# Performance work log

Hardware: AMD Instinct MI355X
Metric: run time of the kernel (lower is better)

Reference implementation:

```python
import jax, jax.numpy as jnp
import numpy as np

PS = 32

def _masks(ps):
    yy, xx = np.meshgrid(np.arange(ps), np.arange(ps), indexing='ij')
    c = (ps - 1) / 2.0
    r = np.sqrt((yy - c) ** 2 + (xx - c) ** 2)
    rm = max(r.max(), 1.0)
    ml = (r <= rm / 3.0).astype(np.float32)
    mm = ((r > rm / 3.0) & (r <= 2.0 * rm / 3.0)).astype(np.float32)
    mh = (r > 2.0 * rm / 3.0).astype(np.float32)
    return jnp.asarray(ml), jnp.asarray(mm), jnp.asarray(mh)

MASK_L, MASK_M, MASK_H = _masks(PS)

def setup_inputs() -> dict:
    key = jax.random.key(0)
    ks = jax.random.split(key, 4)
    B, C, H, W = 16, 3, 256, 256
    d = PS * PS            # 1024
    hidden = int(d * 1.5)  # 1536
    c_f = 64
    return {
        'x': jax.random.normal(ks[0], (B, C, H, W), dtype=jnp.float32),
        'W1': jax.random.normal(ks[1], (d, hidden), dtype=jnp.float32) * 0.02,
        'b1': jnp.zeros((hidden,), jnp.float32),
        'W2': jax.random.normal(ks[2], (hidden, d), dtype=jnp.float32) * 0.02,
        'b2': jnp.zeros((d,), jnp.float32),
        'w_proj': jax.random.normal(ks[3], (c_f,), dtype=jnp.float32) * 0.5,
        'gamma': jnp.ones((c_f,), jnp.float32),
        'beta': jnp.zeros((c_f,), jnp.float32),
        'lf_gate': jnp.float32(0.33),
        'mf_gate': jnp.float32(0.34),
        'hf_gate': jnp.float32(0.33),
    }

def _forward(x, W1, b1, W2, b2, w_proj, gamma, beta, lf_gate, mf_gate, hf_gate):
    B, C, H, W = x.shape
    ps = PS
    gh, gw = H // ps, W // ps
    L = gh * gw
    # grayscale
    xg = 0.299 * x[:, 0] + 0.587 * x[:, 1] + 0.114 * x[:, 2]  # [B,H,W]
    # non-overlapping patchify (H,W multiples of ps -> no padding)
    pr = xg.reshape(B, gh, ps, gw, ps).transpose(0, 1, 3, 2, 4).reshape(B, L, ps, ps)
    # per-patch orthonormal FFT2 and magnitude
    mag = jnp.abs(jnp.fft.fft2(pr, norm='ortho'))  # [B,L,ps,ps]
    gate = (jax.nn.sigmoid(lf_gate) * MASK_L
            + jax.nn.sigmoid(mf_gate) * MASK_M
            + jax.nn.sigmoid(hf_gate) * MASK_H)
    mag = mag * gate
    mag_vec = mag.reshape(B * L, ps * ps)
    attn = jax.nn.sigmoid(jax.nn.relu(mag_vec @ W1 + b1) @ W2 + b2)
    mod = mag_vec * attn
    w = mod.mean(axis=-1).reshape(B, L, 1, 1)  # per-patch scalar weight
    recon = pr * (1.0 + w)
    # fold back (exact inverse of the reshape patchify)
    x_rec = recon.reshape(B, gh, gw, ps, ps).transpose(0, 1, 3, 2, 4).reshape(B, H, W)
    # 1x1 conv (1 -> c_f channels, no bias)
    out = x_rec[:, None, :, :] * w_proj[None, :, None, None]  # [B,c_f,H,W]
    # BatchNorm2d (training mode: batch stats, biased variance)
    mean = out.mean(axis=(0, 2, 3), keepdims=True)
    var = out.var(axis=(0, 2, 3), keepdims=True)
    out = (out - mean) * jax.lax.rsqrt(var + 1e-5)
    out = out * gamma[None, :, None, None] + beta[None, :, None, None]
    return jax.nn.relu(out)

def reference(x, W1, b1, W2, b2, w_proj, gamma, beta, lf_gate, mf_gate, hf_gate):
    return _forward(x, W1, b1, W2, b2, w_proj, gamma, beta, lf_gate, mf_gate, hf_gate)
```

## Files before the change

### kernel.cpp

```cpp
#include <hip/hip_runtime.h>
#include <hip/hip_bf16.h>
#include <math.h>

typedef __attribute__((ext_vector_type(8))) short bf16x8;
typedef __attribute__((ext_vector_type(4))) float f32x4;
typedef __attribute__((ext_vector_type(4))) unsigned short u16x4;

static __device__ __forceinline__ float bf2f(unsigned short u) {
    union { unsigned int i; float f; } v; v.i = ((unsigned int)u) << 16; return v.f;
}
static __device__ __forceinline__ unsigned short f2bf(float f) {
    union { float f; unsigned int i; } v; v.f = f;
    unsigned int x = v.i;
    return (unsigned short)((x + 0x7fffu + ((x >> 16) & 1u)) >> 16);
}
static __device__ __forceinline__ float sigmoidf(float v) {
    return 1.0f / (1.0f + expf(-v));
}

__global__ __launch_bounds__(256) void kpatch(
    const float* __restrict__ x, const float* __restrict__ lf,
    const float* __restrict__ mf, const float* __restrict__ hf,
    float* __restrict__ pr_out, unsigned short* __restrict__ mag_bf)
{
    __shared__ float sX[32][36];
    __shared__ float sYr[32][36];
    __shared__ float sYi[32][36];
    __shared__ float tc[32], ts[32];

    const int t = threadIdx.x;
    const int p = blockIdx.x;
    const int b = p >> 6, l = p & 63;
    const int gy = l >> 3, gx = l & 7;

    if (t < 32) {
        float ang = (float)t * 0.19634954084936207f;
        tc[t] = cosf(ang);
        ts[t] = sinf(ang);
    }

    const int y  = t >> 3;
    const int xc = (t & 7) * 4;
    const int h  = gy * 32 + y;
    const int wbase = gx * 32 + xc;
    const long long idx0 = ((long long)(b * 3 + 0) * 256 + h) * 256 + wbase;
    const long long idx1 = ((long long)(b * 3 + 1) * 256 + h) * 256 + wbase;
    const long long idx2 = ((long long)(b * 3 + 2) * 256 + h) * 256 + wbase;
    float4 r4 = *(const float4*)(x + idx0);
    float4 g4 = *(const float4*)(x + idx1);
    float4 b4 = *(const float4*)(x + idx2);
    float4 gray;
    gray.x = 0.299f * r4.x + 0.587f * g4.x + 0.114f * b4.x;
    gray.y = 0.299f * r4.y + 0.587f * g4.y + 0.114f * b4.y;
    gray.z = 0.299f * r4.z + 0.587f * g4.z + 0.114f * b4.z;
    gray.w = 0.299f * r4.w + 0.587f * g4.w + 0.114f * b4.w;
    *(float4*)&sX[y][xc] = gray;
    *(float4*)(pr_out + p * 1024 + t * 4) = gray;
    __syncthreads();

    {
        const int k  = t >> 3;
        const int c0 = (t & 7) * 4;
        float yr[4] = {0,0,0,0}, yi[4] = {0,0,0,0};
        for (int n = 0; n < 32; n++) {
            int wi = (k * n) & 31;
            float cw = tc[wi], sw = ts[wi];
            float4 xv = *(const float4*)&sX[n][c0];
            yr[0] += cw * xv.x; yi[0] -= sw * xv.x;
            yr[1] += cw * xv.y; yi[1] -= sw * xv.y;
            yr[2] += cw * xv.z; yi[2] -= sw * xv.z;
            yr[3] += cw * xv.w; yi[3] -= sw * xv.w;
        }
        *(float4*)&sYr[k][c0] = *(float4*)yr;
        *(float4*)&sYi[k][c0] = *(float4*)yi;
    }
    __syncthreads();

    {
        const int k  = t >> 3;
        const int m0 = (t & 7) * 4;
        float zr[4] = {0,0,0,0}, zi[4] = {0,0,0,0};
        for (int c = 0; c < 32; c++) {
            float yr = sYr[k][c];
            float yi = sYi[k][c];
            #pragma unroll
            for (int j = 0; j < 4; j++) {
                int wi = ((m0 + j) * c) & 31;
                float cw = tc[wi], sw = ts[wi];
                zr[j] += yr * cw + yi * sw;
                zi[j] += yi * cw - yr * sw;
            }
        }
        const float sl = sigmoidf(lf[0]);
        const float sm = sigmoidf(mf[0]);
        const float sh = sigmoidf(hf[0]);
        const float T1 = 480.5f / 9.0f;
        const float T2 = 4.0f * 480.5f / 9.0f;
        const float fk = (float)k - 15.5f;
        u16x4 outv;
        #pragma unroll
        for (int j = 0; j < 4; j++) {
            float fm = (float)(m0 + j) - 15.5f;
            float r2 = fk * fk + fm * fm;
            float g = (r2 <= T1) ? sl : ((r2 <= T2) ? sm : sh);
            float magv = sqrtf(zr[j] * zr[j] + zi[j] * zi[j]) * 0.03125f * g;
            outv[j] = f2bf(magv);
        }
        *(u16x4*)(mag_bf + p * 1024 + k * 32 + m0) = outv;
    }
}

__global__ __launch_bounds__(256) void kconv(
    const float* __restrict__ W, unsigned short* __restrict__ WT, int K, int N)
{
    __shared__ float tile[32][33];
    const int k0 = blockIdx.x * 32, n0 = blockIdx.y * 32;
    const int tx = threadIdx.x & 31, ty = threadIdx.x >> 5;
    #pragma unroll
    for (int i = 0; i < 4; i++) {
        int r = ty + i * 8;
        tile[r][tx] = W[(long long)(k0 + r) * N + n0 + tx];
    }
    __syncthreads();
    #pragma unroll
    for (int i = 0; i < 4; i++) {
        int r = ty + i * 8;
        WT[(long long)(n0 + r) * K + k0 + tx] = f2bf(tile[tx][r]);
    }
}

__global__ __launch_bounds__(256) void kgemm(
    const unsigned short* __restrict__ A, const unsigned short* __restrict__ BT,
    const float* __restrict__ bias, unsigned short* __restrict__ C,
    int K, int N, int act)
{
    const int lane = threadIdx.x & 63;
    const int wave = threadIdx.x >> 6;
    const int wm = wave & 1, wn = wave >> 1;
    const int m_base = blockIdx.x * 64 + wm * 32;
    const int n_base = blockIdx.y * 64 + wn * 32;
    const int lr = lane & 15;
    const int koff = (lane >> 4) * 8;

    const unsigned short* pa0 = A  + (long long)(m_base + lr) * K + koff;
    const unsigned short* pa1 = pa0 + (long long)16 * K;
    const unsigned short* pb0 = BT + (long long)(n_base + lr) * K + koff;
    const unsigned short* pb1 = pb0 + (long long)16 * K;

    f32x4 acc00 = {0,0,0,0}, acc01 = {0,0,0,0}, acc10 = {0,0,0,0}, acc11 = {0,0,0,0};

    for (int kk = 0; kk < K; kk += 32) {
        bf16x8 a0 = *(const bf16x8*)(pa0 + kk);
        bf16x8 a1 = *(const bf16x8*)(pa1 + kk);
        bf16x8 b0 = *(const bf16x8*)(pb0 + kk);
        bf16x8 b1 = *(const bf16x8*)(pb1 + kk);
        acc00 = __builtin_amdgcn_mfma_f32_16x16x32_bf16(a0, b0, acc00, 0, 0, 0);
        acc01 = __builtin_amdgcn_mfma_f32_16x16x32_bf16(a0, b1, acc01, 0, 0, 0);
        acc10 = __builtin_amdgcn_mfma_f32_16x16x32_bf16(a1, b0, acc10, 0, 0, 0);
        acc11 = __builtin_amdgcn_mfma_f32_16x16x32_bf16(a1, b1, acc11, 0, 0, 0);
    }

    const int quad = lane >> 4;
    const int col0 = n_base + lr, col1 = col0 + 16;
    const float bias0 = bias[col0], bias1 = bias[col1];
    const int row0b = m_base + quad * 4;
    #pragma unroll
    for (int r = 0; r < 4; r++) {
        int row0 = row0b + r, row1 = row0 + 16;
        float v00 = acc00[r] + bias0;
        float v01 = acc01[r] + bias1;
        float v10 = acc10[r] + bias0;
        float v11 = acc11[r] + bias1;
        if (act == 0) {
            v00 = fmaxf(v00, 0.0f); v01 = fmaxf(v01, 0.0f);
            v10 = fmaxf(v10, 0.0f); v11 = fmaxf(v11, 0.0f);
        } else {
            v00 = sigmoidf(v00); v01 = sigmoidf(v01);
            v10 = sigmoidf(v10); v11 = sigmoidf(v11);
        }
        C[(long long)row0 * N + col0] = f2bf(v00);
        C[(long long)row0 * N + col1] = f2bf(v01);
        C[(long long)row1 * N + col0] = f2bf(v10);
        C[(long long)row1 * N + col1] = f2bf(v11);
    }
}

__global__ __launch_bounds__(256) void kmod(
    const unsigned short* __restrict__ mag_bf, const unsigned short* __restrict__ attn_bf,
    const float* __restrict__ pr, float* __restrict__ xrec, float* __restrict__ stats)
{
    __shared__ float red[8];
    __shared__ float sscale;
    const int t = threadIdx.x, p = blockIdx.x;
    const int lane = t & 63, wave = t >> 6;

    u16x4 mv = *(const u16x4*)(mag_bf + p * 1024 + t * 4);
    u16x4 av = *(const u16x4*)(attn_bf + p * 1024 + t * 4);
    float acc = bf2f(mv[0]) * bf2f(av[0]) + bf2f(mv[1]) * bf2f(av[1])
              + bf2f(mv[2]) * bf2f(av[2]) + bf2f(mv[3]) * bf2f(av[3]);
    #pragma unroll
    for (int off = 32; off > 0; off >>= 1) acc += __shfl_down(acc, off, 64);
    if (lane == 0) red[wave] = acc;
    __syncthreads();
    if (t == 0) {
        float s = red[0] + red[1] + red[2] + red[3];
        sscale = 1.0f + s * (1.0f / 1024.0f);
    }
    __syncthreads();
    const float sc = sscale;

    const int b = p >> 6, l = p & 63;
    const int gy = l >> 3, gx = l & 7;
    const int y = t >> 3, xc = (t & 7) * 4;
    float4 pv = *(const float4*)(pr + p * 1024 + t * 4);
    float4 rv;
    rv.x = pv.x * sc; rv.y = pv.y * sc; rv.z = pv.z * sc; rv.w = pv.w * sc;
    *(float4*)(xrec + (long long)b * 65536 + (gy * 32 + y) * 256 + gx * 32 + xc) = rv;

    float ls = rv.x + rv.y + rv.z + rv.w;
    float lq = rv.x * rv.x + rv.y * rv.y + rv.z * rv.z + rv.w * rv.w;
    #pragma unroll
    for (int off = 32; off > 0; off >>= 1) {
        ls += __shfl_down(ls, off, 64);
        lq += __shfl_down(lq, off, 64);
    }
    __syncthreads();
    if (lane == 0) red[wave] = ls;
    __syncthreads();
    float bs = (t == 0) ? (red[0] + red[1] + red[2] + red[3]) : 0.0f;
    __syncthreads();
    if (lane == 0) red[wave] = lq;
    __syncthreads();
    if (t == 0) {
        float bq = red[0] + red[1] + red[2] + red[3];
        atomicAdd(&stats[0], bs);
        atomicAdd(&stats[1], bq);
    }
}

__global__ void kstats(const float* __restrict__ stats, const float* __restrict__ w_proj,
                       const float* __restrict__ gamma, const float* __restrict__ beta,
                       float* __restrict__ der)
{
    const int c = threadIdx.x;
    const float invN = 1.0f / 1048576.0f;
    float mu  = stats[0] * invN;
    float var = stats[1] * invN - mu * mu;
    float wp = w_proj[c];
    float A = wp * gamma[c] / sqrtf(wp * wp * var + 1e-5f);
    der[c]      = A;
    der[64 + c] = beta[c];
    if (c == 0) der[128] = mu;
}

__global__ __launch_bounds__(256) void kout(
    const float* __restrict__ xrec, const float* __restrict__ der, float* __restrict__ out)
{
    const int i4 = blockIdx.x * 256 + threadIdx.x;
    const int plane = i4 >> 14;
    const int c = plane & 63;
    const int b = plane >> 6;
    const float A  = der[c];
    const float be = der[64 + c];
    const float mu = der[128];
    float4 v = ((const float4*)xrec)[b * 16384 + (i4 & 16383)];
    float4 o;
    o.x = fmaxf(fmaf(A, v.x - mu, be), 0.0f);
    o.y = fmaxf(fmaf(A, v.y - mu, be), 0.0f);
    o.z = fmaxf(fmaf(A, v.z - mu, be), 0.0f);
    o.w = fmaxf(fmaf(A, v.w - mu, be), 0.0f);
    ((float4*)out)[i4] = o;
}

extern "C" void kernel_launch(void* const* d_in, const int* in_sizes, int n_in,
                              void* d_out, int out_size, void* d_ws, size_t ws_size,
                              hipStream_t stream)
{
    const float* x      = (const float*)d_in[0];
    const float* W1     = (const float*)d_in[1];
    const float* b1     = (const float*)d_in[2];
    const float* W2     = (const float*)d_in[3];
    const float* b2     = (const float*)d_in[4];
    const float* w_proj = (const float*)d_in[5];
    const float* gamma  = (const float*)d_in[6];
    const float* beta   = (const float*)d_in[7];
    const float* lf     = (const float*)d_in[8];
    const float* mf     = (const float*)d_in[9];
    const float* hf     = (const float*)d_in[10];

    char* ws = (char*)d_ws;
    float* pr                 = (float*)(ws);
    float* xrec               = (float*)(ws + 4194304);
    unsigned short* mag_bf    = (unsigned short*)(ws + 8388608);
    unsigned short* attn_bf   = (unsigned short*)(ws + 10485760);
    unsigned short* hidden_bf = (unsigned short*)(ws + 12582912);
    unsigned short* w1t       = (unsigned short*)(ws + 15728640);
    unsigned short* w2t       = (unsigned short*)(ws + 18874368);
    float* stats              = (float*)(ws + 22020096);
    float* der                = (float*)(ws + 22020224);

    hipMemsetAsync(stats, 0, 8, stream);

    kconv<<<dim3(32, 48), 256, 0, stream>>>(W1, w1t, 1024, 1536);
    kconv<<<dim3(48, 32), 256, 0, stream>>>(W2, w2t, 1536, 1024);
    kpatch<<<1024, 256, 0, stream>>>(x, lf, mf, hf, pr, mag_bf);
    kgemm<<<dim3(16, 24), 256, 0, stream>>>(mag_bf, w1t, b1, hidden_bf, 1024, 1536, 0);
    kgemm<<<dim3(16, 16), 256, 0, stream>>>(hidden_bf, w2t, b2, attn_bf, 1536, 1024, 1);
    kmod<<<1024, 256, 0, stream>>>(mag_bf, attn_bf, pr, xrec, stats);
    kstats<<<1, 64, 0, stream>>>(stats, w_proj, gamma, beta, der);
    kout<<<65536, 256, 0, stream>>>(xrec, der, (float*)d_out);
}
```

Measured before the change: 398.0 us.

## Fuse attention dot-product into GEMM2 epilogue and drop xrec/kmod pass

```diff
diff --git a/kernel.cpp b/kernel.cpp
--- a/kernel.cpp
+++ b/kernel.cpp
@@ -21,17 +21,20 @@
 __global__ __launch_bounds__(256) void kpatch(
     const float* __restrict__ x, const float* __restrict__ lf,
     const float* __restrict__ mf, const float* __restrict__ hf,
-    float* __restrict__ pr_out, unsigned short* __restrict__ mag_bf)
+    float* __restrict__ pr_out, unsigned short* __restrict__ mag_bf,
+    float* __restrict__ ppsum, float* __restrict__ ppsq)
 {
     __shared__ float sX[32][36];
     __shared__ float sYr[32][36];
     __shared__ float sYi[32][36];
     __shared__ float tc[32], ts[32];
+    __shared__ float red_s[4], red_q[4];
 
     const int t = threadIdx.x;
     const int p = blockIdx.x;
     const int b = p >> 6, l = p & 63;
     const int gy = l >> 3, gx = l & 7;
+    const int lane = t & 63, wave = t >> 6;
 
     if (t < 32) {
         float ang = (float)t * 0.19634954084936207f;
@@ -56,7 +59,20 @@
     gray.w = 0.299f * r4.w + 0.587f * g4.w + 0.114f * b4.w;
     *(float4*)&sX[y][xc] = gray;
     *(float4*)(pr_out + p * 1024 + t * 4) = gray;
+
+    float ls = gray.x + gray.y + gray.z + gray.w;
+    float lq = gray.x * gray.x + gray.y * gray.y + gray.z * gray.z + gray.w * gray.w;
+    #pragma unroll
+    for (int off = 32; off > 0; off >>= 1) {
+        ls += __shfl_down(ls, off, 64);
+        lq += __shfl_down(lq, off, 64);
+    }
+    if (lane == 0) { red_s[wave] = ls; red_q[wave] = lq; }
     __syncthreads();
+    if (t == 0) {
+        ppsum[p] = red_s[0] + red_s[1] + red_s[2] + red_s[3];
+        ppsq[p]  = red_q[0] + red_q[1] + red_q[2] + red_q[3];
+    }
 
     {
         const int k  = t >> 3;
@@ -129,11 +145,11 @@
     }
 }
 
-__global__ __launch_bounds__(256) void kgemm(
+__global__ __launch_bounds__(256) void kgemm1(
     const unsigned short* __restrict__ A, const unsigned short* __restrict__ BT,
-    const float* __restrict__ bias, unsigned short* __restrict__ C,
-    int K, int N, int act)
-{
+    const float* __restrict__ bias, unsigned short* __restrict__ C)
+{
+    const int K = 1024, N = 1536;
     const int lane = threadIdx.x & 63;
     const int wave = threadIdx.x >> 6;
     const int wm = wave & 1, wn = wave >> 1;
@@ -167,109 +183,155 @@
     #pragma unroll
     for (int r = 0; r < 4; r++) {
         int row0 = row0b + r, row1 = row0 + 16;
-        float v00 = acc00[r] + bias0;
-        float v01 = acc01[r] + bias1;
-        float v10 = acc10[r] + bias0;
-        float v11 = acc11[r] + bias1;
-        if (act == 0) {
-            v00 = fmaxf(v00, 0.0f); v01 = fmaxf(v01, 0.0f);
-            v10 = fmaxf(v10, 0.0f); v11 = fmaxf(v11, 0.0f);
-        } else {
-            v00 = sigmoidf(v00); v01 = sigmoidf(v01);
-            v10 = sigmoidf(v10); v11 = sigmoidf(v11);
-        }
-        C[(long long)row0 * N + col0] = f2bf(v00);
-        C[(long long)row0 * N + col1] = f2bf(v01);
-        C[(long long)row1 * N + col0] = f2bf(v10);
-        C[(long long)row1 * N + col1] = f2bf(v11);
-    }
-}
-
-__global__ __launch_bounds__(256) void kmod(
-    const unsigned short* __restrict__ mag_bf, const unsigned short* __restrict__ attn_bf,
-    const float* __restrict__ pr, float* __restrict__ xrec, float* __restrict__ stats)
-{
-    __shared__ float red[8];
-    __shared__ float sscale;
-    const int t = threadIdx.x, p = blockIdx.x;
-    const int lane = t & 63, wave = t >> 6;
-
-    u16x4 mv = *(const u16x4*)(mag_bf + p * 1024 + t * 4);
-    u16x4 av = *(const u16x4*)(attn_bf + p * 1024 + t * 4);
-    float acc = bf2f(mv[0]) * bf2f(av[0]) + bf2f(mv[1]) * bf2f(av[1])
-              + bf2f(mv[2]) * bf2f(av[2]) + bf2f(mv[3]) * bf2f(av[3]);
-    #pragma unroll
-    for (int off = 32; off > 0; off >>= 1) acc += __shfl_down(acc, off, 64);
-    if (lane == 0) red[wave] = acc;
+        C[(long long)row0 * N + col0] = f2bf(fmaxf(acc00[r] + bias0, 0.0f));
+        C[(long long)row0 * N + col1] = f2bf(fmaxf(acc01[r] + bias1, 0.0f));
+        C[(long long)row1 * N + col0] = f2bf(fmaxf(acc10[r] + bias0, 0.0f));
+        C[(long long)row1 * N + col1] = f2bf(fmaxf(acc11[r] + bias1, 0.0f));
+    }
+}
+
+__global__ __launch_bounds__(256) void kgemm2d(
+    const unsigned short* __restrict__ A, const unsigned short* __restrict__ BT,
+    const float* __restrict__ bias, const unsigned short* __restrict__ mag,
+    float* __restrict__ wpart)
+{
+    const int K = 1536;
+    const int lane = threadIdx.x & 63;
+    const int wave = threadIdx.x >> 6;
+    const int wm = wave & 1, wn = wave >> 1;
+    const int m_base = blockIdx.x * 64 + wm * 32;
+    const int n_base = blockIdx.y * 64 + wn * 32;
+    const int lr = lane & 15;
+    const int koff = (lane >> 4) * 8;
+
+    const unsigned short* pa0 = A  + (long long)(m_base + lr) * K + koff;
+    const unsigned short* pa1 = pa0 + (long long)16 * K;
+    const unsigned short* pb0 = BT + (long long)(n_base + lr) * K + koff;
+    const unsigned short* pb1 = pb0 + (long long)16 * K;
+
+    f32x4 acc00 = {0,0,0,0}, acc01 = {0,0,0,0}, acc10 = {0,0,0,0}, acc11 = {0,0,0,0};
+
+    for (int kk = 0; kk < K; kk += 32) {
+        bf16x8 a0 = *(const bf16x8*)(pa0 + kk);
+        bf16x8 a1 = *(const bf16x8*)(pa1 + kk);
+        bf16x8 b0 = *(const bf16x8*)(pb0 + kk);
+        bf16x8 b1 = *(const bf16x8*)(pb1 + kk);
+        acc00 = __builtin_amdgcn_mfma_f32_16x16x32_bf16(a0, b0, acc00, 0, 0, 0);
+        acc01 = __builtin_amdgcn_mfma_f32_16x16x32_bf16(a0, b1, acc01, 0, 0, 0);
+        acc10 = __builtin_amdgcn_mfma_f32_16x16x32_bf16(a1, b0, acc10, 0, 0, 0);
+        acc11 = __builtin_amdgcn_mfma_f32_16x16x32_bf16(a1, b1, acc11, 0, 0, 0);
+    }
+
+    const int quad = lane >> 4;
+    const int col0 = n_base + lr, col1 = col0 + 16;
+    const float bias0 = bias[col0], bias1 = bias[col1];
+    const int row0b = m_base + quad * 4;
+
+    float dsum0[4], dsum1[4];
+    #pragma unroll
+    for (int r = 0; r < 4; r++) {
+        int row0 = row0b + r, row1 = row0 + 16;
+        float v00 = sigmoidf(acc00[r] + bias0);
+        float v01 = sigmoidf(acc01[r] + bias1);
+        float v10 = sigmoidf(acc10[r] + bias0);
+        float v11 = sigmoidf(acc11[r] + bias1);
+        float m00 = bf2f(mag[(long long)row0 * 1024 + col0]);
+        float m01 = bf2f(mag[(long long)row0 * 1024 + col1]);
+        float m10 = bf2f(mag[(long long)row1 * 1024 + col0]);
+        float m11 = bf2f(mag[(long long)row1 * 1024 + col1]);
+        dsum0[r] = m00 * v00 + m01 * v01;
+        dsum1[r] = m10 * v10 + m11 * v11;
+    }
+    #pragma unroll
+    for (int r = 0; r < 4; r++) {
+        #pragma unroll
+        for (int mask = 8; mask > 0; mask >>= 1) {
+            dsum0[r] += __shfl_xor(dsum0[r], mask, 64);
+            dsum1[r] += __shfl_xor(dsum1[r], mask, 64);
+        }
+    }
+    if (lr == 0) {
+        const int cp = blockIdx.y * 2 + wn;
+        #pragma unroll
+        for (int r = 0; r < 4; r++) {
+            wpart[(row0b + r) * 32 + cp]      = dsum0[r];
+            wpart[(row0b + 16 + r) * 32 + cp] = dsum1[r];
+        }
+    }
+}
+
+__global__ __launch_bounds__(1024) void kfin(
+    const float* __restrict__ wpart, const float* __restrict__ ppsum,
+    const float* __restrict__ ppsq, const float* __restrict__ w_proj,
+    const float* __restrict__ gamma, const float* __restrict__ beta,
+    float* __restrict__ scales, float* __restrict__ der)
+{
+    __shared__ float rs[16], rq[16];
+    const int p = threadIdx.x;
+    const int lane = p & 63, wave = p >> 6;
+
+    const float4* wp4 = (const float4*)(wpart + p * 32);
+    float w = 0.0f;
+    #pragma unroll
+    for (int j = 0; j < 8; j++) {
+        float4 v = wp4[j];
+        w += v.x + v.y + v.z + v.w;
+    }
+    float scale = 1.0f + w * (1.0f / 1024.0f);
+    scales[p] = scale;
+
+    float s = scale * ppsum[p];
+    float q = scale * scale * ppsq[p];
+    #pragma unroll
+    for (int off = 32; off > 0; off >>= 1) {
+        s += __shfl_down(s, off, 64);
+        q += __shfl_down(q, off, 64);
+    }
+    if (lane == 0) { rs[wave] = s; rq[wave] = q; }
     __syncthreads();
-    if (t == 0) {
-        float s = red[0] + red[1] + red[2] + red[3];
-        sscale = 1.0f + s * (1.0f / 1024.0f);
-    }
-    __syncthreads();
-    const float sc = sscale;
-
-    const int b = p >> 6, l = p & 63;
-    const int gy = l >> 3, gx = l & 7;
-    const int y = t >> 3, xc = (t & 7) * 4;
-    float4 pv = *(const float4*)(pr + p * 1024 + t * 4);
-    float4 rv;
-    rv.x = pv.x * sc; rv.y = pv.y * sc; rv.z = pv.z * sc; rv.w = pv.w * sc;
-    *(float4*)(xrec + (long long)b * 65536 + (gy * 32 + y) * 256 + gx * 32 + xc) = rv;
-
-    float ls = rv.x + rv.y + rv.z + rv.w;
-    float lq = rv.x * rv.x + rv.y * rv.y + rv.z * rv.z + rv.w * rv.w;
-    #pragma unroll
-    for (int off = 32; off > 0; off >>= 1) {
-        ls += __shfl_down(ls, off, 64);
-        lq += __shfl_down(lq, off, 64);
-    }
-    __syncthreads();
-    if (lane == 0) red[wave] = ls;
-    __syncthreads();
-    float bs = (t == 0) ? (red[0] + red[1] + red[2] + red[3]) : 0.0f;
-    __syncthreads();
-    if (lane == 0) red[wave] = lq;
-    __syncthreads();
-    if (t == 0) {
-        float bq = red[0] + red[1] + red[2] + red[3];
-        atomicAdd(&stats[0], bs);
-        atomicAdd(&stats[1], bq);
-    }
-}
-
-__global__ void kstats(const float* __restrict__ stats, const float* __restrict__ w_proj,
-                       const float* __restrict__ gamma, const float* __restrict__ beta,
-                       float* __restrict__ der)
-{
-    const int c = threadIdx.x;
-    const float invN = 1.0f / 1048576.0f;
-    float mu  = stats[0] * invN;
-    float var = stats[1] * invN - mu * mu;
-    float wp = w_proj[c];
-    float A = wp * gamma[c] / sqrtf(wp * wp * var + 1e-5f);
-    der[c]      = A;
-    der[64 + c] = beta[c];
-    if (c == 0) der[128] = mu;
+    if (p < 64) {
+        float S = (p < 16) ? rs[p] : 0.0f;
+        float Q = (p < 16) ? rq[p] : 0.0f;
+        #pragma unroll
+        for (int off = 8; off > 0; off >>= 1) {
+            S += __shfl_down(S, off, 64);
+            Q += __shfl_down(Q, off, 64);
+        }
+        S = __shfl(S, 0, 64);
+        Q = __shfl(Q, 0, 64);
+        const float invN = 1.0f / 1048576.0f;
+        float mu  = S * invN;
+        float var = Q * invN - mu * mu;
+        float wp = w_proj[p];
+        float A = wp * gamma[p] / sqrtf(wp * wp * var + 1e-5f);
+        der[p]      = A;
+        der[64 + p] = beta[p] - A * mu;
+    }
 }
 
 __global__ __launch_bounds__(256) void kout(
-    const float* __restrict__ xrec, const float* __restrict__ der, float* __restrict__ out)
-{
-    const int i4 = blockIdx.x * 256 + threadIdx.x;
-    const int plane = i4 >> 14;
-    const int c = plane & 63;
-    const int b = plane >> 6;
-    const float A  = der[c];
-    const float be = der[64 + c];
-    const float mu = der[128];
-    float4 v = ((const float4*)xrec)[b * 16384 + (i4 & 16383)];
-    float4 o;
-    o.x = fmaxf(fmaf(A, v.x - mu, be), 0.0f);
-    o.y = fmaxf(fmaf(A, v.y - mu, be), 0.0f);
-    o.z = fmaxf(fmaf(A, v.z - mu, be), 0.0f);
-    o.w = fmaxf(fmaf(A, v.w - mu, be), 0.0f);
-    ((float4*)out)[i4] = o;
+    const float* __restrict__ pr, const float* __restrict__ scales,
+    const float* __restrict__ der, float* __restrict__ out)
+{
+    const int total4 = 16777216;
+    for (int i4 = blockIdx.x * 256 + threadIdx.x; i4 < total4; i4 += gridDim.x * 256) {
+        const int w4 = i4 & 63;
+        const int h = (i4 >> 6) & 255;
+        const int plane = i4 >> 14;
+        const int c = plane & 63;
+        const int b = plane >> 6;
+        const int p = (b << 6) + ((h >> 5) << 3) + (w4 >> 3);
+        const int off4 = ((h & 31) << 3) + (w4 & 7);
+        const float As = der[c] * scales[p];
+        const float D2 = der[64 + c];
+        float4 v = ((const float4*)pr)[p * 256 + off4];
+        float4 o;
+        o.x = fmaxf(fmaf(As, v.x, D2), 0.0f);
+        o.y = fmaxf(fmaf(As, v.y, D2), 0.0f);
+        o.z = fmaxf(fmaf(As, v.z, D2), 0.0f);
+        o.w = fmaxf(fmaf(As, v.w, D2), 0.0f);
+        ((float4*)out)[i4] = o;
+    }
 }
 
 extern "C" void kernel_launch(void* const* d_in, const int* in_sizes, int n_in,
@@ -290,23 +352,21 @@
 
     char* ws = (char*)d_ws;
     float* pr                 = (float*)(ws);
-    float* xrec               = (float*)(ws + 4194304);
-    unsigned short* mag_bf    = (unsigned short*)(ws + 8388608);
-    unsigned short* attn_bf   = (unsigned short*)(ws + 10485760);
-    unsigned short* hidden_bf = (unsigned short*)(ws + 12582912);
-    unsigned short* w1t       = (unsigned short*)(ws + 15728640);
-    unsigned short* w2t       = (unsigned short*)(ws + 18874368);
-    float* stats              = (float*)(ws + 22020096);
-    float* der                = (float*)(ws + 22020224);
-
-    hipMemsetAsync(stats, 0, 8, stream);
+    unsigned short* mag_bf    = (unsigned short*)(ws + (4u<<20));
+    unsigned short* hidden_bf = (unsigned short*)(ws + (6u<<20));
+    unsigned short* w1t       = (unsigned short*)(ws + (10u<<20));
+    unsigned short* w2t       = (unsigned short*)(ws + (13u<<20));
+    float* wpart              = (float*)(ws + (16u<<20));
+    float* ppsum              = (float*)(ws + (17u<<20));
+    float* ppsq               = (float*)(ws + (17u<<20) + 4096);
+    float* scales             = (float*)(ws + (17u<<20) + 8192);
+    float* der                = (float*)(ws + (17u<<20) + 12288);
 
     kconv<<<dim3(32, 48), 256, 0, stream>>>(W1, w1t, 1024, 1536);
     kconv<<<dim3(48, 32), 256, 0, stream>>>(W2, w2t, 1536, 1024);
-    kpatch<<<1024, 256, 0, stream>>>(x, lf, mf, hf, pr, mag_bf);
-    kgemm<<<dim3(16, 24), 256, 0, stream>>>(mag_bf, w1t, b1, hidden_bf, 1024, 1536, 0);
-    kgemm<<<dim3(16, 16), 256, 0, stream>>>(hidden_bf, w2t, b2, attn_bf, 1536, 1024, 1);
-    kmod<<<1024, 256, 0, stream>>>(mag_bf, attn_bf, pr, xrec, stats);
-    kstats<<<1, 64, 0, stream>>>(stats, w_proj, gamma, beta, der);
-    kout<<<65536, 256, 0, stream>>>(xrec, der, (float*)d_out);
-}
+    kpatch<<<1024, 256, 0, stream>>>(x, lf, mf, hf, pr, mag_bf, ppsum, ppsq);
+    kgemm1<<<dim3(16, 24), 256, 0, stream>>>(mag_bf, w1t, b1, hidden_bf);
+    kgemm2d<<<dim3(16, 16), 256, 0, stream>>>(hidden_bf, w2t, b2, mag_bf, wpart);
+    kfin<<<1, 1024, 0, stream>>>(wpart, ppsum, ppsq, w_proj, gamma, beta, scales, der);
+    kout<<<2048, 256, 0, stream>>>(pr, scales, der, (float*)d_out);
+}
```

After: 385.0 us. 1.03x faster.
